# Kernel tuning notes

Measured on AMD Instinct MI355X. Metric: run time of the kernel, lower is better.

Reference implementation:

```python
import jax, jax.numpy as jnp
import numpy as np

N, E, B = 16384, 131072, 256
F_IN, HID, HEADS, F_CELL, N_OUT = 78, 128, 10, 954, 2
NEG_SLOPE = 0.2  # PyG GATConv default


def setup_inputs() -> dict:
    key = jax.random.key(0)
    ks = jax.random.split(key, 24)
    rn = lambda k, shape, s=0.05: (jax.random.normal(k, shape, jnp.float32) * s)
    inp = {
        "x": rn(ks[0], (N, F_IN), 1.0),
        "edge_index": jax.random.randint(ks[1], (2, E), 0, N, dtype=jnp.int32),
        "batch": (jnp.arange(N, dtype=jnp.int32) // (N // B)),  # 64 nodes per graph, sorted
        "cell": rn(ks[2], (B, F_CELL), 1.0),
        "W1": rn(ks[3], (F_IN, HEADS * HID)),
        "a_src1": rn(ks[4], (HEADS, HID)),
        "a_dst1": rn(ks[5], (HEADS, HID)),
        "b1": jnp.zeros((HEADS * HID,), jnp.float32),
        # GATConv layer 2: 1280 -> 128, 1 head
        "W2": rn(ks[6], (HEADS * HID, HID)),
        "a_src2": rn(ks[7], (1, HID)),
        "a_dst2": rn(ks[8], (1, HID)),
        "b2": jnp.zeros((HID,), jnp.float32),
        # drug1_fc_g1: 128 -> 128
        "Wg": rn(ks[9], (HID, HID)), "bg": jnp.zeros((HID,), jnp.float32),
        # fc head applied to normalized cell (source applies fc1 to cell: 954 -> 2048)
        "Wf1": rn(ks[10], (F_CELL, 2048)), "bf1": jnp.zeros((2048,), jnp.float32),
        "Wf2": rn(ks[11], (2048, 512)), "bf2": jnp.zeros((512,), jnp.float32),
        "Wf3": rn(ks[12], (512, 128)), "bf3": jnp.zeros((128,), jnp.float32),
        "Wo": rn(ks[13], (128, N_OUT)), "bo": jnp.zeros((N_OUT,), jnp.float32),
    }
    return inp


def _gat_layer(xin, src, dst, W, a_s, a_d, b, heads, ch):
    """PyG GATConv: linear -> per-edge leaky_relu(a_src.h_j + a_dst.h_i) ->
    segment softmax over incoming edges of dst -> scatter-add of alpha * h_src."""
    n = xin.shape[0]
    h = (xin @ W).reshape(n, heads, ch)                       # [N,H,C]
    es = jnp.einsum('nhc,hc->nh', h, a_s)                     # alpha_src per node
    ed = jnp.einsum('nhc,hc->nh', h, a_d)                     # alpha_dst per node
    e = jax.nn.leaky_relu(es[src] + ed[dst], NEG_SLOPE)       # [Etot,H]
    m = jax.ops.segment_max(e, dst, num_segments=n)           # stable softmax max
    w = jnp.exp(e - m[dst])                                   # unnormalized alpha
    denom = jax.ops.segment_sum(w, dst, num_segments=n)       # [N,H]
    num = jax.ops.segment_sum(w[:, :, None] * h[src], dst, num_segments=n)  # [N,H,C]
    out = num / denom[:, :, None]
    return out.reshape(n, heads * ch) + b


def reference(x, edge_index, batch, cell, W1, a_src1, a_dst1, b1,
              W2, a_src2, a_dst2, b2, Wg, bg, Wf1, bf1, Wf2, bf2,
              Wf3, bf3, Wo, bo):
    n = x.shape[0]
    # add self-loops (PyG GATConv default)
    loop = jnp.arange(n, dtype=edge_index.dtype)
    src = jnp.concatenate([edge_index[0], loop])
    dst = jnp.concatenate([edge_index[1], loop])

    x1 = jax.nn.elu(_gat_layer(x, src, dst, W1, a_src1, a_dst1, b1, HEADS, HID))
    x1 = jax.nn.elu(_gat_layer(x1, src, dst, W2, a_src2, a_dst2, b2, 1, HID))
    # global max pool over graphs (batch is sorted, all B segments non-empty)
    x1 = jax.ops.segment_max(x1, batch, num_segments=B)       # [B,128]
    x1 = jax.nn.relu(x1 @ Wg + bg)

    # cell branch: L2 normalize rows, then dense head (dropout = identity in eval)
    celln = cell / jnp.maximum(jnp.linalg.norm(cell, axis=1, keepdims=True), 1e-12)
    xc = jax.nn.relu(celln @ Wf1 + bf1)
    xc = jax.nn.relu(xc @ Wf2 + bf2)
    xc = jax.nn.relu(xc @ Wf3 + bf3)
    out = xc @ Wo + bo                                        # [B,2]
    # source returns only `out`; we also expose the (otherwise-dead) GAT branch
    return jnp.concatenate([x1, out], axis=1)                 # [B,130]
```

## Files before the change

### kernel.cpp

```cpp
#include <hip/hip_runtime.h>
#include <hip/hip_bf16.h>
#include <math.h>

#define N_NODES 16384
#define E_EDGES 131072
#define ETOT (E_EDGES + N_NODES)
#define BGRAPH 256
#define F_INPUT 78
#define KPAD1 96
#define HID 128
#define HEADS 10
#define F1 (HEADS * HID)
#define F_CELL 954
#define KPADC 960
#define NEG_SLOPE 0.2f

typedef __attribute__((ext_vector_type(8))) short frag_t;
typedef __attribute__((ext_vector_type(4))) float f4_t;

static __device__ __forceinline__ unsigned fkey(float f) {
    unsigned b = __float_as_uint(f);
    return (b & 0x80000000u) ? ~b : (b | 0x80000000u);
}
static __device__ __forceinline__ float funkey(unsigned k) {
    unsigned b = (k & 0x80000000u) ? (k ^ 0x80000000u) : ~k;
    return __uint_as_float(b);
}
static __device__ __forceinline__ unsigned short f2bf(float f) {
    __hip_bfloat16 h = __float2bfloat16(f);
    return *(unsigned short*)&h;
}
static __device__ __forceinline__ float bf2f(unsigned short u) {
    return __uint_as_float(((unsigned)u) << 16);
}

template<int WM16, int WN16, int OUT_MODE, int ACT, int HAS_BIAS>
__global__ __launch_bounds__(256) void mfma_gemm(
    const unsigned short* __restrict__ A, const unsigned short* __restrict__ BT,
    const float* __restrict__ bias, void* __restrict__ C,
    float* __restrict__ esp, float* __restrict__ edp,
    const float* __restrict__ ca, const float* __restrict__ cd,
    int M, int N, int Kpad, int lda, int ldb, int ldc,
    int za, int zb, int zc, int zbias)
{
    constexpr int BM = 32 * WM16, BN = 32 * WN16;
    __shared__ __align__(16) unsigned short Als[BM * 32];
    __shared__ __align__(16) unsigned short Bls[BN * 32];
    const int z = blockIdx.z;
    A  += (size_t)z * za;
    BT += (size_t)z * zb;
    const int t = threadIdx.x;
    const int wave = t >> 6, lane = t & 63;
    const int wr = (wave >> 1) * (16 * WM16);
    const int wc = (wave & 1) * (16 * WN16);
    const int row0 = blockIdx.y * BM;
    const int col0 = blockIdx.x * BN;

    f4_t acc[WM16][WN16];
#pragma unroll
    for (int m = 0; m < WM16; m++)
#pragma unroll
        for (int n = 0; n < WN16; n++) { acc[m][n] = (f4_t){0.f, 0.f, 0.f, 0.f}; }

    const int lrow = lane & 15, kg = lane >> 4;
    for (int kk = 0; kk < Kpad; kk += 32) {
        for (int i = t; i < BM * 4; i += 256) {
            int r = i >> 2, slot = i & 3;
            uint4 v = *(const uint4*)&A[(size_t)(row0 + r) * lda + kk + slot * 8];
            *(uint4*)&Als[r * 32 + ((slot ^ (r & 3) ^ ((r >> 2) & 3)) * 8)] = v;
        }
        for (int i = t; i < BN * 4; i += 256) {
            int r = i >> 2, slot = i & 3;
            uint4 v = *(const uint4*)&BT[(size_t)(col0 + r) * ldb + kk + slot * 8];
            *(uint4*)&Bls[r * 32 + ((slot ^ (r & 3) ^ ((r >> 2) & 3)) * 8)] = v;
        }
        __syncthreads();
        frag_t af[WM16], bfr[WN16];
#pragma unroll
        for (int m = 0; m < WM16; m++) {
            int r = wr + m * 16 + lrow;
            af[m] = *(frag_t*)&Als[r * 32 + ((kg ^ (r & 3) ^ ((r >> 2) & 3)) * 8)];
        }
#pragma unroll
        for (int n = 0; n < WN16; n++) {
            int r = wc + n * 16 + lrow;
            bfr[n] = *(frag_t*)&Bls[r * 32 + ((kg ^ (r & 3) ^ ((r >> 2) & 3)) * 8)];
        }
#pragma unroll
        for (int m = 0; m < WM16; m++)
#pragma unroll
            for (int n = 0; n < WN16; n++)
                acc[m][n] = __builtin_amdgcn_mfma_f32_16x16x32_bf16(af[m], bfr[n], acc[m][n], 0, 0, 0);
        __syncthreads();
    }

    if constexpr (OUT_MODE <= 2) {
#pragma unroll
        for (int m = 0; m < WM16; m++) {
#pragma unroll
            for (int n = 0; n < WN16; n++) {
                int col = col0 + wc + n * 16 + lrow;
                float bv = HAS_BIAS ? bias[z * zbias + col] : 0.f;
#pragma unroll
                for (int r = 0; r < 4; r++) {
                    int row = row0 + wr + m * 16 + kg * 4 + r;
                    float v = acc[m][n][r] + bv;
                    if (ACT == 1) v = fmaxf(v, 0.f);
                    if (ACT == 2) v = (v > 0.f) ? v : expm1f(v);
                    size_t ci = (size_t)row * ldc + (size_t)z * zc + col;
                    if (OUT_MODE == 0)      ((float*)C)[ci] = v;
                    else if (OUT_MODE == 1) ((unsigned short*)C)[ci] = f2bf(v);
                    else {
                        if (col < 10)                  esp[row * 10 + col] = v;
                        else if (col >= 16 && col < 26) edp[row * 10 + (col - 16)] = v;
                    }
                }
            }
        }
    } else {
        __shared__ float o2l[BM][2];
        if (t < BM) { o2l[t][0] = 0.f; o2l[t][1] = 0.f; }
        __syncthreads();
#pragma unroll
        for (int m = 0; m < WM16; m++) {
#pragma unroll
            for (int r = 0; r < 4; r++) {
                int lr = wr + m * 16 + kg * 4 + r;
                float p0 = 0.f, p1 = 0.f;
#pragma unroll
                for (int n = 0; n < WN16; n++) {
                    int col = col0 + wc + n * 16 + lrow;
                    float v = acc[m][n][r] + (HAS_BIAS ? bias[col] : 0.f);
                    if (ACT == 1) v = fmaxf(v, 0.f);
                    p0 = fmaf(v, ca[col * 2], p0);
                    p1 = fmaf(v, ca[col * 2 + 1], p1);
                }
                atomicAdd(&o2l[lr][0], p0);
                atomicAdd(&o2l[lr][1], p1);
            }
        }
        __syncthreads();
        if (t < BM) {
            ((float*)C)[(size_t)(row0 + t) * ldc + 128] = o2l[t][0] + cd[0];
            ((float*)C)[(size_t)(row0 + t) * ldc + 129] = o2l[t][1] + cd[1];
        }
    }
}

__global__ __launch_bounds__(256) void h2_gemm(
    const unsigned short* __restrict__ A, const unsigned short* __restrict__ BT,
    unsigned short* __restrict__ C)
{
    __shared__ __align__(16) unsigned short Als[2][32 * 32];
    __shared__ __align__(16) unsigned short Bls[2][128 * 32];
    const int t = threadIdx.x;
    const int wave = t >> 6, lane = t & 63;
    const int lrow = lane & 15, kg = lane >> 4;
    const int row0 = blockIdx.x * 32;
    const int wc = wave * 32;

    const int ar = t >> 2, asl = t & 3;
    const int br = t >> 2, bsl = t & 3;

    uint4 pa, pb0, pb1;
    auto LOAD = [&](int kk) {
        if (t < 128) pa = *(const uint4*)&A[(size_t)(row0 + ar) * F1 + kk + asl * 8];
        pb0 = *(const uint4*)&BT[(size_t)br * F1 + kk + bsl * 8];
        pb1 = *(const uint4*)&BT[(size_t)(br + 64) * F1 + kk + bsl * 8];
    };
    auto STORE = [&](int buf) {
        if (t < 128)
            *(uint4*)&Als[buf][ar * 32 + ((asl ^ (ar & 3) ^ ((ar >> 2) & 3)) * 8)] = pa;
        *(uint4*)&Bls[buf][br * 32 + ((bsl ^ (br & 3) ^ ((br >> 2) & 3)) * 8)] = pb0;
        int r2 = br + 64;
        *(uint4*)&Bls[buf][r2 * 32 + ((bsl ^ (r2 & 3) ^ ((r2 >> 2) & 3)) * 8)] = pb1;
    };

    LOAD(0);
    STORE(0);
    __syncthreads();

    f4_t acc[2][2];
#pragma unroll
    for (int m = 0; m < 2; m++)
#pragma unroll
        for (int n = 0; n < 2; n++) acc[m][n] = (f4_t){0.f, 0.f, 0.f, 0.f};

    int cur = 0;
    for (int ks = 0; ks < 40; ks++) {
        if (ks < 39) LOAD((ks + 1) * 32);
        frag_t af[2], bfr[2];
#pragma unroll
        for (int m = 0; m < 2; m++) {
            int r = m * 16 + lrow;
            af[m] = *(frag_t*)&Als[cur][r * 32 + ((kg ^ (r & 3) ^ ((r >> 2) & 3)) * 8)];
        }
#pragma unroll
        for (int n = 0; n < 2; n++) {
            int r = wc + n * 16 + lrow;
            bfr[n] = *(frag_t*)&Bls[cur][r * 32 + ((kg ^ (r & 3) ^ ((r >> 2) & 3)) * 8)];
        }
#pragma unroll
        for (int m = 0; m < 2; m++)
#pragma unroll
            for (int n = 0; n < 2; n++)
                acc[m][n] = __builtin_amdgcn_mfma_f32_16x16x32_bf16(af[m], bfr[n], acc[m][n], 0, 0, 0);
        if (ks < 39) STORE(cur ^ 1);
        __syncthreads();
        cur ^= 1;
    }

#pragma unroll
    for (int m = 0; m < 2; m++) {
#pragma unroll
        for (int n = 0; n < 2; n++) {
            int col = wc + n * 16 + lrow;
#pragma unroll
            for (int r = 0; r < 4; r++) {
                int row = row0 + m * 16 + kg * 4 + r;
                C[(size_t)row * HID + col] = f2bf(acc[m][n][r]);
            }
        }
    }
}

#define S0 1572864
#define S1 122880
#define S2 163840
#define S3 1966080
#define S4 1048576
#define S5 65536
#define S6 16384
#define PREP_TOTAL (S0+S1+S2+S3+S4+S5+S6)
#define NB_ELEM (PREP_TOTAL / 256)
#define NB_FOLD 768
#define NB_ZCNT 64
#define NB_ZPK  128

__global__ void prep_all(const float* __restrict__ x,  const float* __restrict__ W1,
                         const float* __restrict__ W2, const float* __restrict__ Wf1,
                         const float* __restrict__ Wf2, const float* __restrict__ Wf3,
                         const float* __restrict__ Wg,
                         const float* __restrict__ as1, const float* __restrict__ ad1,
                         unsigned short* __restrict__ xb,  unsigned short* __restrict__ W1T,
                         unsigned short* __restrict__ W2T, unsigned short* __restrict__ Wf1T,
                         unsigned short* __restrict__ Wf2T, unsigned short* __restrict__ Wf3T,
                         unsigned short* __restrict__ WgT, unsigned short* __restrict__ F1T,
                         int* __restrict__ counts, unsigned* __restrict__ pk)
{
    int blk = blockIdx.x, t = threadIdx.x;
    if (blk < NB_ELEM) {
        int i = blk * 256 + t;
        if (i < S0) { int r = i / 96, k = i % 96;
            xb[i] = (k < F_INPUT) ? f2bf(x[r * F_INPUT + k]) : 0; return; }
        i -= S0;
        if (i < S1) { int n = i / 96, k = i % 96;
            W1T[i] = (k < F_INPUT) ? f2bf(W1[(size_t)k * F1 + n]) : 0; return; }
        i -= S1;
        if (i < S2) { int n = i / 1280, k = i % 1280;
            W2T[i] = f2bf(W2[(size_t)k * HID + n]); return; }
        i -= S2;
        if (i < S3) { int n = i / 960, k = i % 960;
            Wf1T[i] = (k < F_CELL) ? f2bf(Wf1[(size_t)k * 2048 + n]) : 0; return; }
        i -= S3;
        if (i < S4) { int n = i / 2048, k = i % 2048;
            Wf2T[i] = f2bf(Wf2[(size_t)k * 512 + n]); return; }
        i -= S4;
        if (i < S5) { int n = i / 512, k = i % 512;
            Wf3T[i] = f2bf(Wf3[(size_t)k * HID + n]); return; }
        i -= S5;
        { int n = i / 128, k = i % 128;
            WgT[i] = f2bf(Wg[(size_t)k * HID + n]); }
        return;
    }
    blk -= NB_ELEM;
    if (blk < NB_FOLD) {
        int idx = blk * 4 + (t >> 6);
        int l = t & 63;
        int r = idx / 96, k = idx % 96;
        int sd = r >> 4, h = r & 15;
        float p = 0.f;
        if (h < HEADS && k < F_INPUT) {
            const float* a = (sd ? ad1 : as1) + h * HID;
            float2 wv = *(const float2*)&W1[(size_t)k * F1 + h * HID + 2 * l];
            float2 av = *(const float2*)&a[2 * l];
            p = wv.x * av.x + wv.y * av.y;
#pragma unroll
            for (int o = 32; o > 0; o >>= 1) p += __shfl_xor(p, o);
        }
        if (l == 0) F1T[(size_t)r * 96 + k] = f2bf(p);
        return;
    }
    blk -= NB_FOLD;
    if (blk < NB_ZCNT) { counts[blk * 256 + t] = 0; return; }
    blk -= NB_ZCNT;
    pk[blk * 256 + t] = 0;
}

__global__ void hist_dst(const int* __restrict__ ei, int* __restrict__ counts)
{
    int e = blockIdx.x * blockDim.x + threadIdx.x;
    if (e >= ETOT) return;
    int dst = (e < E_EDGES) ? ei[E_EDGES + e] : (e - E_EDGES);
    atomicAdd(&counts[dst], 1);
}

__global__ void scan_counts(const int* __restrict__ counts,
                            int* __restrict__ row_start, int* __restrict__ cursor)
{
    __shared__ int part[256];
    int t = threadIdx.x;
    int base = t * 64;
    int sum = 0;
    for (int i = 0; i < 64; i++) sum += counts[base + i];
    part[t] = sum;
    __syncthreads();
    for (int o = 1; o < 256; o <<= 1) {
        int v = 0;
        if (t >= o) v = part[t - o];
        __syncthreads();
        part[t] += v;
        __syncthreads();
    }
    int run = (t == 0) ? 0 : part[t - 1];
    for (int i = 0; i < 64; i++) {
        row_start[base + i] = run;
        cursor[base + i] = run;
        run += counts[base + i];
    }
    if (t == 255) row_start[N_NODES] = run;
}

__global__ void scatter_csr(const int* __restrict__ ei, int* __restrict__ cursor,
                            int* __restrict__ csr_src)
{
    int e = blockIdx.x * blockDim.x + threadIdx.x;
    if (e >= ETOT) return;
    int src, dst;
    if (e < E_EDGES) { src = ei[e]; dst = ei[E_EDGES + e]; } else { src = dst = e - E_EDGES; }
    int pos = atomicAdd(&cursor[dst], 1);
    csr_src[pos] = src;
}

__global__ void h2_coef(const unsigned short* __restrict__ H2,
                        const float* __restrict__ as_, const float* __restrict__ ad_,
                        float* __restrict__ es, float* __restrict__ ed)
{
    int n = blockIdx.x * 4 + (threadIdx.x >> 6);
    int l = threadIdx.x & 63;
    unsigned p = *(const unsigned*)&H2[(size_t)n * HID + 2 * l];
    float h0 = bf2f((unsigned short)(p & 0xffffu));
    float h1 = bf2f((unsigned short)(p >> 16));
    float2 av = *(const float2*)&as_[2 * l];
    float2 dv = *(const float2*)&ad_[2 * l];
    float vs = h0 * av.x + h1 * av.y;
    float vd = h0 * dv.x + h1 * dv.y;
#pragma unroll
    for (int o = 32; o > 0; o >>= 1) { vs += __shfl_xor(vs, o); vd += __shfl_xor(vd, o); }
    if (l == 0) { es[n] = vs; ed[n] = vd; }
}

__global__ __launch_bounds__(256) void gat1_agg(
    const int* __restrict__ row_start, const int* __restrict__ csr_src,
    const unsigned* __restrict__ xb32,
    const float* __restrict__ es, const float* __restrict__ ed,
    unsigned* __restrict__ aggb)
{
    const int w = threadIdx.x >> 6, l = threadIdx.x & 63;
    const int n = blockIdx.x * 4 + w;
    const int rs = row_start[n];
    const int deg = row_start[n + 1] - rs;

    __shared__ __align__(16) float w_lds[4][64][12];
    __shared__ int src_lds[4][64];

    float edv[HEADS];
    const float* edp = ed + n * HEADS;
#pragma unroll
    for (int h = 0; h < HEADS; h++) edv[h] = edp[h];

    float acc0[HEADS], acc1[HEADS], den[HEADS];
#pragma unroll
    for (int h = 0; h < HEADS; h++) { acc0[h] = 0.f; acc1[h] = 0.f; den[h] = 0.f; }

    for (int base = 0; base < deg; base += 64) {
        int e = base + l;
        int cnt = min(64, deg - base);
        float wv[HEADS];
        if (e < deg) {
            int s = csr_src[rs + e];
            src_lds[w][l] = s;
            const float* ep = es + s * HEADS;
#pragma unroll
            for (int h = 0; h < HEADS; h++) {
                float v = ep[h] + edv[h];
                v = (v >= 0.f) ? v : NEG_SLOPE * v;
                wv[h] = __expf(v);
            }
        } else {
#pragma unroll
            for (int h = 0; h < HEADS; h++) wv[h] = 0.f;
        }
#pragma unroll
        for (int h = 0; h < HEADS; h++) {
            den[h] += wv[h];
            w_lds[w][l][h] = wv[h];
        }
        asm volatile("" ::: "memory");

        for (int j = 0; j < cnt; j++) {
            int sj = src_lds[w][j];
            unsigned xv = 0;
            if (l < 48) xv = xb32[(size_t)sj * 48 + l];
            float x0 = bf2f((unsigned short)(xv & 0xffffu));
            float x1v = bf2f((unsigned short)(xv >> 16));
            float4 wa = *(const float4*)&w_lds[w][j][0];
            float4 wb = *(const float4*)&w_lds[w][j][4];
            float2 wcv = *(const float2*)&w_lds[w][j][8];
            float ww[HEADS] = {wa.x, wa.y, wa.z, wa.w, wb.x, wb.y, wb.z, wb.w, wcv.x, wcv.y};
#pragma unroll
            for (int h = 0; h < HEADS; h++) {
                acc0[h] = fmaf(ww[h], x0, acc0[h]);
                acc1[h] = fmaf(ww[h], x1v, acc1[h]);
            }
        }
        asm volatile("" ::: "memory");
    }

#pragma unroll
    for (int h = 0; h < HEADS; h++)
#pragma unroll
        for (int o = 32; o > 0; o >>= 1) den[h] += __shfl_xor(den[h], o);

    if (l < 48) {
        unsigned* orow = aggb + (size_t)n * 480;
#pragma unroll
        for (int h = 0; h < HEADS; h++) {
            float inv = 1.f / den[h];
            unsigned lo = f2bf(acc0[h] * inv);
            unsigned hi = f2bf(acc1[h] * inv);
            orow[h * 48 + l] = lo | (hi << 16);
        }
    }
}

__global__ __launch_bounds__(256) void gat2_agg(
    const int* __restrict__ row_start, const int* __restrict__ csr_src,
    const unsigned short* __restrict__ H2,
    const float* __restrict__ es, const float* __restrict__ ed,
    const float* __restrict__ b, const int* __restrict__ batch,
    unsigned* __restrict__ pk)
{
    const int w = threadIdx.x >> 6, l = threadIdx.x & 63;
    const int n = blockIdx.x * 4 + w;
    const int rs = row_start[n];
    const int deg = row_start[n + 1] - rs;
    const float edv = ed[n];

    float2 acc = {0.f, 0.f};
    float den = 0.f;
    for (int base = 0; base < deg; base += 64) {
        int e = base + l;
        int cnt = min(64, deg - base);
        int s = 0;
        float wv = 0.f;
        if (e < deg) {
            s = csr_src[rs + e];
            float v = es[s] + edv;
            v = (v >= 0.f) ? v : NEG_SLOPE * v;
            wv = __expf(v);
        }
        den += wv;
        for (int j = 0; j < cnt; j++) {
            float wj = __shfl(wv, j);
            int   sj = __shfl(s, j);
            unsigned hp = *(const unsigned*)&H2[(size_t)sj * HID + 2 * l];
            acc.x = fmaf(wj, bf2f((unsigned short)(hp & 0xffffu)), acc.x);
            acc.y = fmaf(wj, bf2f((unsigned short)(hp >> 16)), acc.y);
        }
    }
#pragma unroll
    for (int o = 32; o > 0; o >>= 1) den += __shfl_xor(den, o);

    float inv = 1.f / den;
    float2 bv = *(const float2*)&b[2 * l];
    float v0 = acc.x * inv + bv.x;
    float v1 = acc.y * inv + bv.y;
    v0 = (v0 > 0.f) ? v0 : expm1f(v0);
    v1 = (v1 > 0.f) ? v1 : expm1f(v1);
    int g = batch[n];
    atomicMax(&pk[g * HID + 2 * l], fkey(v0));
    atomicMax(&pk[g * HID + 2 * l + 1], fkey(v1));
}

__global__ void decode_cell(const unsigned* __restrict__ pk,
                            unsigned short* __restrict__ pooledb,
                            const float* __restrict__ cell,
                            unsigned short* __restrict__ celln)
{
    int t = threadIdx.x;
    if (blockIdx.x < BGRAPH) {
        int b = blockIdx.x;
        __shared__ float red[256];
        float s = 0.f;
        for (int c = t; c < F_CELL; c += 256) { float v = cell[(size_t)b * F_CELL + c]; s += v * v; }
        red[t] = s; __syncthreads();
        for (int o = 128; o > 0; o >>= 1) { if (t < o) red[t] += red[t + o]; __syncthreads(); }
        float inv = 1.f / fmaxf(sqrtf(red[0]), 1e-12f);
        for (int c = t; c < KPADC; c += 256) {
            float v = (c < F_CELL) ? cell[(size_t)b * F_CELL + c] * inv : 0.f;
            celln[(size_t)b * KPADC + c] = f2bf(v);
        }
    } else {
        int i = (blockIdx.x - BGRAPH) * 256 + t;
        if (i < BGRAPH * HID) pooledb[i] = f2bf(funkey(pk[i]));
    }
}

extern "C" void kernel_launch(void* const* d_in, const int* in_sizes, int n_in,
                              void* d_out, int out_size, void* d_ws, size_t ws_size,
                              hipStream_t stream)
{
    const float* x    = (const float*)d_in[0];
    const int*   ei   = (const int*)d_in[1];
    const int*   batch= (const int*)d_in[2];
    const float* cell = (const float*)d_in[3];
    const float* W1   = (const float*)d_in[4];
    const float* as1  = (const float*)d_in[5];
    const float* ad1  = (const float*)d_in[6];
    const float* b1   = (const float*)d_in[7];
    const float* W2   = (const float*)d_in[8];
    const float* as2  = (const float*)d_in[9];
    const float* ad2  = (const float*)d_in[10];
    const float* b2   = (const float*)d_in[11];
    const float* Wg   = (const float*)d_in[12];
    const float* bg   = (const float*)d_in[13];
    const float* Wf1  = (const float*)d_in[14];
    const float* bf1  = (const float*)d_in[15];
    const float* Wf2  = (const float*)d_in[16];
    const float* bf2  = (const float*)d_in[17];
    const float* Wf3  = (const float*)d_in[18];
    const float* bf3  = (const float*)d_in[19];
    const float* Wo   = (const float*)d_in[20];
    const float* bo   = (const float*)d_in[21];
    float* out = (float*)d_out;

    char* w = (char*)d_ws;
    auto alloc = [&](size_t bytes) { char* p = w; w += (bytes + 255) & ~(size_t)255; return p; };
    unsigned short* xb   = (unsigned short*)alloc((size_t)N_NODES * KPAD1 * 2);
    unsigned short* W1T  = (unsigned short*)alloc((size_t)F1 * KPAD1 * 2);
    unsigned short* F1T  = (unsigned short*)alloc((size_t)32 * KPAD1 * 2);
    unsigned*       aggb = (unsigned*)alloc((size_t)N_NODES * 480 * 4);
    unsigned short* x1   = (unsigned short*)alloc((size_t)N_NODES * F1 * 2);
    unsigned short* W2T  = (unsigned short*)alloc((size_t)HID * F1 * 2);
    unsigned short* H2   = (unsigned short*)alloc((size_t)N_NODES * HID * 2);
    float*    es1  = (float*)alloc((size_t)N_NODES * HEADS * 4);
    float*    ed1  = (float*)alloc((size_t)N_NODES * HEADS * 4);
    float*    es2  = (float*)alloc((size_t)N_NODES * 4);
    float*    ed2  = (float*)alloc((size_t)N_NODES * 4);
    int*      counts    = (int*)alloc((size_t)N_NODES * 4);
    int*      row_start = (int*)alloc((size_t)(N_NODES + 1) * 4);
    int*      cursor    = (int*)alloc((size_t)N_NODES * 4);
    int*      csr_src   = (int*)alloc((size_t)ETOT * 4);
    unsigned* pk   = (unsigned*)alloc((size_t)BGRAPH * HID * 4);
    unsigned short* pooledb = (unsigned short*)alloc((size_t)BGRAPH * HID * 2);
    unsigned short* WgT  = (unsigned short*)alloc((size_t)HID * HID * 2);
    unsigned short* celln = (unsigned short*)alloc((size_t)BGRAPH * KPADC * 2);
    unsigned short* Wf1T = (unsigned short*)alloc((size_t)2048 * KPADC * 2);
    unsigned short* Wf2T = (unsigned short*)alloc((size_t)512 * 2048 * 2);
    unsigned short* Wf3T = (unsigned short*)alloc((size_t)HID * 512 * 2);
    unsigned short* xc1b = (unsigned short*)alloc((size_t)BGRAPH * 2048 * 2);
    unsigned short* xc2b = (unsigned short*)alloc((size_t)BGRAPH * 512 * 2);

    dim3 b256(256);
    const int egrid = (ETOT + 255) / 256;

    prep_all<<<NB_ELEM + NB_FOLD + NB_ZCNT + NB_ZPK, b256, 0, stream>>>(
        x, W1, W2, Wf1, Wf2, Wf3, Wg, as1, ad1,
        xb, W1T, W2T, Wf1T, Wf2T, Wf3T, WgT, F1T, counts, pk);

    hist_dst<<<egrid, b256, 0, stream>>>(ei, counts);
    scan_counts<<<1, b256, 0, stream>>>(counts, row_start, cursor);
    scatter_csr<<<egrid, b256, 0, stream>>>(ei, cursor, csr_src);

    mfma_gemm<4, 1, 2, 0, 0><<<dim3(1, N_NODES / 128), b256, 0, stream>>>(
        xb, F1T, nullptr, nullptr, es1, ed1, nullptr, nullptr,
        N_NODES, 32, KPAD1, KPAD1, KPAD1, 32, 0, 0, 0, 0);

    gat1_agg<<<N_NODES / 4, b256, 0, stream>>>(row_start, csr_src, (const unsigned*)xb,
                                               es1, ed1, aggb);

    mfma_gemm<4, 4, 1, 2, 1><<<dim3(1, N_NODES / 128, HEADS), b256, 0, stream>>>(
        (const unsigned short*)aggb, W1T, b1, x1, nullptr, nullptr, nullptr, nullptr,
        N_NODES, HID, KPAD1, 960, KPAD1, F1, KPAD1, HID * KPAD1, HID, HID);

    h2_gemm<<<N_NODES / 32, b256, 0, stream>>>(x1, W2T, H2);

    h2_coef<<<N_NODES / 4, b256, 0, stream>>>(H2, as2, ad2, es2, ed2);

    gat2_agg<<<N_NODES / 4, b256, 0, stream>>>(row_start, csr_src, H2, es2, ed2, b2,
                                               batch, pk);

    decode_cell<<<BGRAPH + (BGRAPH * HID + 255) / 256, b256, 0, stream>>>(
        pk, pooledb, cell, celln);

    mfma_gemm<2, 2, 0, 1, 1><<<dim3(HID / 64, BGRAPH / 64), b256, 0, stream>>>(
        pooledb, WgT, bg, out, nullptr, nullptr, nullptr, nullptr,
        BGRAPH, HID, HID, HID, HID, 130, 0, 0, 0, 0);

    mfma_gemm<2, 2, 1, 1, 1><<<dim3(2048 / 64, BGRAPH / 64), b256, 0, stream>>>(
        celln, Wf1T, bf1, xc1b, nullptr, nullptr, nullptr, nullptr,
        BGRAPH, 2048, KPADC, KPADC, KPADC, 2048, 0, 0, 0, 0);
    mfma_gemm<1, 2, 1, 1, 1><<<dim3(512 / 64, BGRAPH / 32), b256, 0, stream>>>(
        xc1b, Wf2T, bf2, xc2b, nullptr, nullptr, nullptr, nullptr,
        BGRAPH, 512, 2048, 2048, 2048, 512, 0, 0, 0, 0);

    mfma_gemm<2, 4, 4, 1, 1><<<dim3(1, BGRAPH / 64), b256, 0, stream>>>(
        xc2b, Wf3T, bf3, out, nullptr, nullptr, Wo, bo,
        BGRAPH, HID, 512, 512, 512, 130, 0, 0, 0, 0);
}
```

Measured before the change: 232.1 us.

## Double-buffer GEMMs, fuse h2 coefficients, merge histogram into prep, vectorize scan

Adds a register-prefetched, double-buffered GEMM kernel and uses it for the GAT layer-1 GEMMs and the first two cell MLP layers, with smaller tiles for some of them. The es2/ed2 attention coefficients are now computed in the h2_gemm epilogue through shuffle reductions, which removes the separate h2_coef kernel. The destination histogram is folded into prep_all, and counts are zeroed with hipMemsetAsync instead. The scan reads and writes with int4 vectors. Together these cut launch count and memory round-trips, at the cost of more registers and LDS in the double-buffered kernel.

Measured after the change: 243.9 us. 1.05x slower.

```diff
diff --git a/kernel.cpp b/kernel.cpp
--- a/kernel.cpp
+++ b/kernel.cpp
@@ -35,17 +35,20 @@
 }
 
 template<int WM16, int WN16, int OUT_MODE, int ACT, int HAS_BIAS>
-__global__ __launch_bounds__(256) void mfma_gemm(
+__global__ __launch_bounds__(256) void gemm_db(
     const unsigned short* __restrict__ A, const unsigned short* __restrict__ BT,
     const float* __restrict__ bias, void* __restrict__ C,
     float* __restrict__ esp, float* __restrict__ edp,
-    const float* __restrict__ ca, const float* __restrict__ cd,
-    int M, int N, int Kpad, int lda, int ldb, int ldc,
+    int M, int N, int K, int lda, int ldb, int ldc,
     int za, int zb, int zc, int zbias)
 {
     constexpr int BM = 32 * WM16, BN = 32 * WN16;
-    __shared__ __align__(16) unsigned short Als[BM * 32];
-    __shared__ __align__(16) unsigned short Bls[BN * 32];
+    constexpr int LA = BM * 4;
+    constexpr int LB = BN * 4;
+    constexpr int NA = (LA + 255) / 256;
+    constexpr int NB = (LB + 255) / 256;
+    __shared__ __align__(16) unsigned short Als[2][BM * 32];
+    __shared__ __align__(16) unsigned short Bls[2][BN * 32];
     const int z = blockIdx.z;
     A  += (size_t)z * za;
     BT += (size_t)z * zb;
@@ -55,6 +58,105 @@
     const int wc = (wave & 1) * (16 * WN16);
     const int row0 = blockIdx.y * BM;
     const int col0 = blockIdx.x * BN;
+    const int lrow = lane & 15, kg = lane >> 4;
+
+    uint4 pa[NA], pb[NB];
+    auto LOAD = [&](int kk) {
+#pragma unroll
+        for (int i = 0; i < NA; i++) { int idx = t + i * 256; if (idx < LA) {
+            int r = idx >> 2, sl = idx & 3;
+            pa[i] = *(const uint4*)&A[(size_t)(row0 + r) * lda + kk + sl * 8]; } }
+#pragma unroll
+        for (int i = 0; i < NB; i++) { int idx = t + i * 256; if (idx < LB) {
+            int r = idx >> 2, sl = idx & 3;
+            pb[i] = *(const uint4*)&BT[(size_t)(col0 + r) * ldb + kk + sl * 8]; } }
+    };
+    auto STORE = [&](int buf) {
+#pragma unroll
+        for (int i = 0; i < NA; i++) { int idx = t + i * 256; if (idx < LA) {
+            int r = idx >> 2, sl = idx & 3;
+            *(uint4*)&Als[buf][r * 32 + ((sl ^ (r & 3) ^ ((r >> 2) & 3)) * 8)] = pa[i]; } }
+#pragma unroll
+        for (int i = 0; i < NB; i++) { int idx = t + i * 256; if (idx < LB) {
+            int r = idx >> 2, sl = idx & 3;
+            *(uint4*)&Bls[buf][r * 32 + ((sl ^ (r & 3) ^ ((r >> 2) & 3)) * 8)] = pb[i]; } }
+    };
+
+    f4_t acc[WM16][WN16];
+#pragma unroll
+    for (int m = 0; m < WM16; m++)
+#pragma unroll
+        for (int n = 0; n < WN16; n++) acc[m][n] = (f4_t){0.f, 0.f, 0.f, 0.f};
+
+    LOAD(0);
+    STORE(0);
+    __syncthreads();
+
+    const int nk = K / 32;
+    int cur = 0;
+    for (int ks = 0; ks < nk; ks++) {
+        if (ks < nk - 1) LOAD((ks + 1) * 32);
+        frag_t af[WM16], bfr[WN16];
+#pragma unroll
+        for (int m = 0; m < WM16; m++) {
+            int r = wr + m * 16 + lrow;
+            af[m] = *(frag_t*)&Als[cur][r * 32 + ((kg ^ (r & 3) ^ ((r >> 2) & 3)) * 8)];
+        }
+#pragma unroll
+        for (int n = 0; n < WN16; n++) {
+            int r = wc + n * 16 + lrow;
+            bfr[n] = *(frag_t*)&Bls[cur][r * 32 + ((kg ^ (r & 3) ^ ((r >> 2) & 3)) * 8)];
+        }
+#pragma unroll
+        for (int m = 0; m < WM16; m++)
+#pragma unroll
+            for (int n = 0; n < WN16; n++)
+                acc[m][n] = __builtin_amdgcn_mfma_f32_16x16x32_bf16(af[m], bfr[n], acc[m][n], 0, 0, 0);
+        if (ks < nk - 1) STORE(cur ^ 1);
+        __syncthreads();
+        cur ^= 1;
+    }
+
+#pragma unroll
+    for (int m = 0; m < WM16; m++) {
+#pragma unroll
+        for (int n = 0; n < WN16; n++) {
+            int col = col0 + wc + n * 16 + lrow;
+            float bv = HAS_BIAS ? bias[z * zbias + col] : 0.f;
+#pragma unroll
+            for (int r = 0; r < 4; r++) {
+                int row = row0 + wr + m * 16 + kg * 4 + r;
+                float v = acc[m][n][r] + bv;
+                if (ACT == 1) v = fmaxf(v, 0.f);
+                if (ACT == 2) v = (v > 0.f) ? v : expm1f(v);
+                size_t ci = (size_t)row * ldc + (size_t)z * zc + col;
+                if (OUT_MODE == 0)      ((float*)C)[ci] = v;
+                else if (OUT_MODE == 1) ((unsigned short*)C)[ci] = f2bf(v);
+                else {
+                    if (col < 10)                  esp[row * 10 + col] = v;
+                    else if (col >= 16 && col < 26) edp[row * 10 + (col - 16)] = v;
+                }
+            }
+        }
+    }
+}
+
+template<int WM16, int WN16, int OUT_MODE, int ACT, int HAS_BIAS>
+__global__ __launch_bounds__(256) void mfma_gemm(
+    const unsigned short* __restrict__ A, const unsigned short* __restrict__ BT,
+    const float* __restrict__ bias, void* __restrict__ C,
+    const float* __restrict__ ca, const float* __restrict__ cd,
+    int M, int N, int Kpad, int lda, int ldb, int ldc)
+{
+    constexpr int BM = 32 * WM16, BN = 32 * WN16;
+    __shared__ __align__(16) unsigned short Als[BM * 32];
+    __shared__ __align__(16) unsigned short Bls[BN * 32];
+    const int t = threadIdx.x;
+    const int wave = t >> 6, lane = t & 63;
+    const int wr = (wave >> 1) * (16 * WM16);
+    const int wc = (wave & 1) * (16 * WN16);
+    const int row0 = blockIdx.y * BM;
+    const int col0 = blockIdx.x * BN;
 
     f4_t acc[WM16][WN16];
 #pragma unroll
@@ -94,26 +196,19 @@
         __syncthreads();
     }
 
-    if constexpr (OUT_MODE <= 2) {
+    if constexpr (OUT_MODE == 0) {
 #pragma unroll
         for (int m = 0; m < WM16; m++) {
 #pragma unroll
             for (int n = 0; n < WN16; n++) {
                 int col = col0 + wc + n * 16 + lrow;
-                float bv = HAS_BIAS ? bias[z * zbias + col] : 0.f;
+                float bv = HAS_BIAS ? bias[col] : 0.f;
 #pragma unroll
                 for (int r = 0; r < 4; r++) {
                     int row = row0 + wr + m * 16 + kg * 4 + r;
                     float v = acc[m][n][r] + bv;
                     if (ACT == 1) v = fmaxf(v, 0.f);
-                    if (ACT == 2) v = (v > 0.f) ? v : expm1f(v);
-                    size_t ci = (size_t)row * ldc + (size_t)z * zc + col;
-                    if (OUT_MODE == 0)      ((float*)C)[ci] = v;
-                    else if (OUT_MODE == 1) ((unsigned short*)C)[ci] = f2bf(v);
-                    else {
-                        if (col < 10)                  esp[row * 10 + col] = v;
-                        else if (col >= 16 && col < 26) edp[row * 10 + (col - 16)] = v;
-                    }
+                    ((float*)C)[(size_t)row * ldc + col] = v;
                 }
             }
         }
@@ -149,10 +244,13 @@
 
 __global__ __launch_bounds__(256) void h2_gemm(
     const unsigned short* __restrict__ A, const unsigned short* __restrict__ BT,
-    unsigned short* __restrict__ C)
+    unsigned short* __restrict__ C,
+    const float* __restrict__ as2, const float* __restrict__ ad2,
+    float* __restrict__ es2, float* __restrict__ ed2)
 {
     __shared__ __align__(16) unsigned short Als[2][32 * 32];
     __shared__ __align__(16) unsigned short Bls[2][128 * 32];
+    __shared__ float esl[4][32], edl[4][32];
     const int t = threadIdx.x;
     const int wave = t >> 6, lane = t & 63;
     const int lrow = lane & 15, kg = lane >> 4;
@@ -213,14 +311,29 @@
 #pragma unroll
     for (int m = 0; m < 2; m++) {
 #pragma unroll
-        for (int n = 0; n < 2; n++) {
-            int col = wc + n * 16 + lrow;
-#pragma unroll
-            for (int r = 0; r < 4; r++) {
-                int row = row0 + m * 16 + kg * 4 + r;
-                C[(size_t)row * HID + col] = f2bf(acc[m][n][r]);
+        for (int r = 0; r < 4; r++) {
+            int lr = m * 16 + kg * 4 + r;
+            float pes = 0.f, ped = 0.f;
+#pragma unroll
+            for (int n = 0; n < 2; n++) {
+                int col = wc + n * 16 + lrow;
+                float v = acc[m][n][r];
+                C[(size_t)(row0 + lr) * HID + col] = f2bf(v);
+                pes = fmaf(v, as2[col], pes);
+                ped = fmaf(v, ad2[col], ped);
             }
-        }
+#pragma unroll
+            for (int o = 1; o < 16; o <<= 1) {
+                pes += __shfl_xor(pes, o);
+                ped += __shfl_xor(ped, o);
+            }
+            if (lrow == 0) { esl[wave][lr] = pes; edl[wave][lr] = ped; }
+        }
+    }
+    __syncthreads();
+    if (t < 32) {
+        es2[row0 + t] = esl[0][t] + esl[1][t] + esl[2][t] + esl[3][t];
+        ed2[row0 + t] = edl[0][t] + edl[1][t] + edl[2][t] + edl[3][t];
     }
 }
 
@@ -234,14 +347,15 @@
 #define PREP_TOTAL (S0+S1+S2+S3+S4+S5+S6)
 #define NB_ELEM (PREP_TOTAL / 256)
 #define NB_FOLD 768
-#define NB_ZCNT 64
 #define NB_ZPK  128
+#define NB_HIST ((ETOT + 255) / 256)
 
 __global__ void prep_all(const float* __restrict__ x,  const float* __restrict__ W1,
                          const float* __restrict__ W2, const float* __restrict__ Wf1,
                          const float* __restrict__ Wf2, const float* __restrict__ Wf3,
                          const float* __restrict__ Wg,
                          const float* __restrict__ as1, const float* __restrict__ ad1,
+                         const int* __restrict__ ei,
                          unsigned short* __restrict__ xb,  unsigned short* __restrict__ W1T,
                          unsigned short* __restrict__ W2T, unsigned short* __restrict__ Wf1T,
                          unsigned short* __restrict__ Wf2T, unsigned short* __restrict__ Wf3T,
@@ -292,17 +406,13 @@
         return;
     }
     blk -= NB_FOLD;
-    if (blk < NB_ZCNT) { counts[blk * 256 + t] = 0; return; }
-    blk -= NB_ZCNT;
-    pk[blk * 256 + t] = 0;
-}
-
-__global__ void hist_dst(const int* __restrict__ ei, int* __restrict__ counts)
-{
-    int e = blockIdx.x * blockDim.x + threadIdx.x;
-    if (e >= ETOT) return;
-    int dst = (e < E_EDGES) ? ei[E_EDGES + e] : (e - E_EDGES);
-    atomicAdd(&counts[dst], 1);
+    if (blk < NB_ZPK) { pk[blk * 256 + t] = 0; return; }
+    blk -= NB_ZPK;
+    int e = blk * 256 + t;
+    if (e < ETOT) {
+        int dst = (e < E_EDGES) ? ei[E_EDGES + e] : (e - E_EDGES);
+        atomicAdd(&counts[dst], 1);
+    }
 }
 
 __global__ void scan_counts(const int* __restrict__ counts,
@@ -311,22 +421,30 @@
     __shared__ int part[256];
     int t = threadIdx.x;
     int base = t * 64;
+    int4 v[16];
+#pragma unroll
+    for (int i = 0; i < 16; i++) v[i] = *(const int4*)&counts[base + i * 4];
     int sum = 0;
-    for (int i = 0; i < 64; i++) sum += counts[base + i];
+#pragma unroll
+    for (int i = 0; i < 16; i++) sum += v[i].x + v[i].y + v[i].z + v[i].w;
     part[t] = sum;
     __syncthreads();
     for (int o = 1; o < 256; o <<= 1) {
-        int v = 0;
-        if (t >= o) v = part[t - o];
+        int vv = (t >= o) ? part[t - o] : 0;
         __syncthreads();
-        part[t] += v;
+        part[t] += vv;
         __syncthreads();
     }
     int run = (t == 0) ? 0 : part[t - 1];
-    for (int i = 0; i < 64; i++) {
-        row_start[base + i] = run;
-        cursor[base + i] = run;
-        run += counts[base + i];
+#pragma unroll
+    for (int i = 0; i < 16; i++) {
+        int4 w;
+        w.x = run; run += v[i].x;
+        w.y = run; run += v[i].y;
+        w.z = run; run += v[i].z;
+        w.w = run; run += v[i].w;
+        *(int4*)&row_start[base + i * 4] = w;
+        *(int4*)&cursor[base + i * 4] = w;
     }
     if (t == 255) row_start[N_NODES] = run;
 }
@@ -340,24 +458,6 @@
     if (e < E_EDGES) { src = ei[e]; dst = ei[E_EDGES + e]; } else { src = dst = e - E_EDGES; }
     int pos = atomicAdd(&cursor[dst], 1);
     csr_src[pos] = src;
-}
-
-__global__ void h2_coef(const unsigned short* __restrict__ H2,
-                        const float* __restrict__ as_, const float* __restrict__ ad_,
-                        float* __restrict__ es, float* __restrict__ ed)
-{
-    int n = blockIdx.x * 4 + (threadIdx.x >> 6);
-    int l = threadIdx.x & 63;
-    unsigned p = *(const unsigned*)&H2[(size_t)n * HID + 2 * l];
-    float h0 = bf2f((unsigned short)(p & 0xffffu));
-    float h1 = bf2f((unsigned short)(p >> 16));
-    float2 av = *(const float2*)&as_[2 * l];
-    float2 dv = *(const float2*)&ad_[2 * l];
-    float vs = h0 * av.x + h1 * av.y;
-    float vd = h0 * dv.x + h1 * dv.y;
-#pragma unroll
-    for (int o = 32; o > 0; o >>= 1) { vs += __shfl_xor(vs, o); vd += __shfl_xor(vd, o); }
-    if (l == 0) { es[n] = vs; ed[n] = vd; }
 }
 
 __global__ __launch_bounds__(256) void gat1_agg(
@@ -573,30 +673,28 @@
     unsigned short* xc2b = (unsigned short*)alloc((size_t)BGRAPH * 512 * 2);
 
     dim3 b256(256);
-    const int egrid = (ETOT + 255) / 256;
-
-    prep_all<<<NB_ELEM + NB_FOLD + NB_ZCNT + NB_ZPK, b256, 0, stream>>>(
-        x, W1, W2, Wf1, Wf2, Wf3, Wg, as1, ad1,
+
+    hipMemsetAsync(counts, 0, (size_t)N_NODES * 4, stream);
+
+    prep_all<<<NB_ELEM + NB_FOLD + NB_ZPK + NB_HIST, b256, 0, stream>>>(
+        x, W1, W2, Wf1, Wf2, Wf3, Wg, as1, ad1, ei,
         xb, W1T, W2T, Wf1T, Wf2T, Wf3T, WgT, F1T, counts, pk);
 
-    hist_dst<<<egrid, b256, 0, stream>>>(ei, counts);
     scan_counts<<<1, b256, 0, stream>>>(counts, row_start, cursor);
-    scatter_csr<<<egrid, b256, 0, stream>>>(ei, cursor, csr_src);
-
-    mfma_gemm<4, 1, 2, 0, 0><<<dim3(1, N_NODES / 128), b256, 0, stream>>>(
-        xb, F1T, nullptr, nullptr, es1, ed1, nullptr, nullptr,
+    scatter_csr<<<(ETOT + 255) / 256, b256, 0, stream>>>(ei, cursor, csr_src);
+
+    gemm_db<2, 1, 2, 0, 0><<<dim3(1, N_NODES / 64), b256, 0, stream>>>(
+        xb, F1T, nullptr, nullptr, es1, ed1,
         N_NODES, 32, KPAD1, KPAD1, KPAD1, 32, 0, 0, 0, 0);
 
     gat1_agg<<<N_NODES / 4, b256, 0, stream>>>(row_start, csr_src, (const unsigned*)xb,
                                                es1, ed1, aggb);
 
-    mfma_gemm<4, 4, 1, 2, 1><<<dim3(1, N_NODES / 128, HEADS), b256, 0, stream>>>(
-        (const unsigned short*)aggb, W1T, b1, x1, nullptr, nullptr, nullptr, nullptr,
+    gemm_db<4, 4, 1, 2, 1><<<dim3(1, N_NODES / 128, HEADS), b256, 0, stream>>>(
+        (const unsigned short*)aggb, W1T, b1, x1, nullptr, nullptr,
         N_NODES, HID, KPAD1, 960, KPAD1, F1, KPAD1, HID * KPAD1, HID, HID);
 
-    h2_gemm<<<N_NODES / 32, b256, 0, stream>>>(x1, W2T, H2);
-
-    h2_coef<<<N_NODES / 4, b256, 0, stream>>>(H2, as2, ad2, es2, ed2);
+    h2_gemm<<<N_NODES / 32, b256, 0, stream>>>(x1, W2T, H2, as2, ad2, es2, ed2);
 
     gat2_agg<<<N_NODES / 4, b256, 0, stream>>>(row_start, csr_src, H2, es2, ed2, b2,
                                                batch, pk);
@@ -605,17 +703,17 @@
         pk, pooledb, cell, celln);
 
     mfma_gemm<2, 2, 0, 1, 1><<<dim3(HID / 64, BGRAPH / 64), b256, 0, stream>>>(
-        pooledb, WgT, bg, out, nullptr, nullptr, nullptr, nullptr,
-        BGRAPH, HID, HID, HID, HID, 130, 0, 0, 0, 0);
-
-    mfma_gemm<2, 2, 1, 1, 1><<<dim3(2048 / 64, BGRAPH / 64), b256, 0, stream>>>(
-        celln, Wf1T, bf1, xc1b, nullptr, nullptr, nullptr, nullptr,
+        pooledb, WgT, bg, out, nullptr, nullptr,
+        BGRAPH, HID, HID, HID, HID, 130);
+
+    gemm_db<1, 2, 1, 1, 1><<<dim3(2048 / 64, BGRAPH / 32), b256, 0, stream>>>(
+        celln, Wf1T, bf1, xc1b, nullptr, nullptr,
         BGRAPH, 2048, KPADC, KPADC, KPADC, 2048, 0, 0, 0, 0);
-    mfma_gemm<1, 2, 1, 1, 1><<<dim3(512 / 64, BGRAPH / 32), b256, 0, stream>>>(
-        xc1b, Wf2T, bf2, xc2b, nullptr, nullptr, nullptr, nullptr,
+    gemm_db<1, 2, 1, 1, 1><<<dim3(512 / 64, BGRAPH / 32), b256, 0, stream>>>(
+        xc1b, Wf2T, bf2, xc2b, nullptr, nullptr,
         BGRAPH, 512, 2048, 2048, 2048, 512, 0, 0, 0, 0);
 
     mfma_gemm<2, 4, 4, 1, 1><<<dim3(1, BGRAPH / 64), b256, 0, stream>>>(
-        xc2b, Wf3T, bf3, out, nullptr, nullptr, Wo, bo,
-        BGRAPH, HID, 512, 512, 512, 130, 0, 0, 0, 0);
-}
+        xc2b, Wf3T, bf3, out, Wo, bo,
+        BGRAPH, HID, 512, 512, 512, 130);
+}
```
